# Performance work log

Measured on AMD Instinct MI355X. Metric: run time of the kernel, lower is better.

Reference implementation:

```python
import jax, jax.numpy as jnp
import numpy as np

N_KERNELS = 5
MUL_FACTOR = 2.0


def setup_inputs() -> dict:
    key = jax.random.key(0)
    k1, k2 = jax.random.split(key)
    x = jax.random.normal(k1, (8192, 64), dtype=jnp.float32)
    y = jax.random.normal(k2, (8192, 64), dtype=jnp.float32)
    return {"x": x, "y": y}


def reference(x, y):
    # bandwidth multipliers: mul_factor ** (arange(n) - n//2) -> [0.25,0.5,1,2,4]
    mults = MUL_FACTOR ** (jnp.arange(N_KERNELS, dtype=jnp.float32) - N_KERNELS // 2)

    z = jnp.concatenate([x, y], axis=0)  # [N, d], N = n + m
    n = x.shape[0]
    N = z.shape[0]

    # squared pairwise L2 distances: ||a||^2 + ||b||^2 - 2 a.b, clamped at 0
    sq = jnp.sum(z * z, axis=-1)  # [N]
    d2 = jnp.maximum(sq[:, None] + sq[None, :] - 2.0 * (z @ z.T), 0.0)  # [N, N]

    # data-dependent bandwidth: sum(d2) / (N^2 - N)
    bw = jnp.sum(d2) / (N * N - N)

    # multi-bandwidth RBF kernel, summed over kernels: [N, N]
    K = jnp.sum(jnp.exp(-d2[None, :, :] / (bw * mults)[:, None, None]), axis=0)

    XX = jnp.mean(K[:n, :n])
    XY = jnp.mean(K[:n, n:])
    YY = jnp.mean(K[n:, n:])
    return XX - 2.0 * XY + YY
```

## Files before the change

### kernel.cpp

```cpp
#include <hip/hip_runtime.h>
#include <hip/hip_bf16.h>

#define D 64

typedef __attribute__((ext_vector_type(8))) _Float16 half8;
typedef __attribute__((ext_vector_type(4))) float floatx4;
typedef __attribute__((ext_vector_type(2))) float f32x2;

typedef __attribute__((address_space(1))) unsigned int gu32_t;
typedef __attribute__((address_space(3))) unsigned int lu32_t;

__global__ __launch_bounds__(256) void k_pre(const float* __restrict__ x, const float* __restrict__ y,
                                             int nx, _Float16* __restrict__ zh,
                                             float* __restrict__ sq, double* __restrict__ Tpart,
                                             float* __restrict__ Spart) {
    int tid = threadIdx.x;
    int lane = tid & 63, wid = tid >> 6;
    int t = blockIdx.x * 256 + tid;
    size_t e = (size_t)t * 8;
    int row = (int)(e >> 6);
    const float* src = (row < nx) ? (x + e) : (y + (e - (size_t)nx * D));
    float4 v0 = ((const float4*)src)[0];
    float4 v1 = ((const float4*)src)[1];
    half8 h;
    h[0]=(_Float16)v0.x; h[1]=(_Float16)v0.y; h[2]=(_Float16)v0.z; h[3]=(_Float16)v0.w;
    h[4]=(_Float16)v1.x; h[5]=(_Float16)v1.y; h[6]=(_Float16)v1.z; h[7]=(_Float16)v1.w;
    *(half8*)(zh + e) = h;
    float p = v0.x*v0.x + v0.y*v0.y + v0.z*v0.z + v0.w*v0.w
            + v1.x*v1.x + v1.y*v1.y + v1.z*v1.z + v1.w*v1.w;
    float s = p;
    s += __shfl_xor(s, 1);
    s += __shfl_xor(s, 2);
    s += __shfl_xor(s, 4);
    if ((tid & 7) == 0) sq[row] = s;

    __shared__ float colbuf[32][64];
    int rib = tid >> 3, cg = tid & 7;
    *(float4*)&colbuf[rib][cg * 8]     = v0;
    *(float4*)&colbuf[rib][cg * 8 + 4] = v1;

    double dp = (double)p;
    dp += __shfl_xor(dp, 1);
    dp += __shfl_xor(dp, 2);
    dp += __shfl_xor(dp, 4);
    dp += __shfl_xor(dp, 8);
    dp += __shfl_xor(dp, 16);
    dp += __shfl_xor(dp, 32);
    __shared__ double redw[4];
    if (lane == 0) redw[wid] = dp;
    __syncthreads();
    if (tid == 0) Tpart[blockIdx.x] = (redw[0] + redw[1]) + (redw[2] + redw[3]);

    if (tid < 64) {
        float cs = 0.f;
#pragma unroll
        for (int r2 = 0; r2 < 32; ++r2) cs += colbuf[r2][tid];
        Spart[blockIdx.x * 64 + tid] = cs;
    }
}

__global__ __launch_bounds__(256) void k_bw(const double* __restrict__ Tpart, int ntp,
                                            const float* __restrict__ Spart, int nsp,
                                            int N, float* __restrict__ cq_p) {
    int t = threadIdx.x;
    double Tp = 0.0;
    for (int b = t; b < ntp; b += 256) Tp += Tpart[b];

    int q = t >> 6, col = t & 63;
    int bpq = nsp >> 2;
    const float* sp = Spart + (size_t)(q * bpq) * 64 + col;
    float c0 = 0.f, c1 = 0.f, c2 = 0.f, c3 = 0.f;
    for (int b = 0; b < bpq; b += 4) {
        c0 += sp[(b + 0) * 64];
        c1 += sp[(b + 1) * 64];
        c2 += sp[(b + 2) * 64];
        c3 += sp[(b + 3) * 64];
    }
    __shared__ float cred[256];
    cred[t] = (c0 + c1) + (c2 + c3);

    __shared__ double red[256];
    red[t] = Tp;
    __syncthreads();
    for (int off = 128; off > 0; off >>= 1) {
        if (t < off) red[t] += red[t + off];
        __syncthreads();
    }
    double T = red[0];
    __shared__ double red2[64];
    if (t < 64) {
        float Sk = cred[t] + cred[t + 64] + cred[t + 128] + cred[t + 192];
        red2[t] = (double)Sk * (double)Sk;
    }
    __syncthreads();
    if (t == 0) {
        double S2 = 0.0;
        for (int i = 0; i < 64; ++i) S2 += red2[i];
        double sumd2 = 2.0 * (double)N * T - 2.0 * S2;
        double bw = sumd2 / ((double)N * (double)N - (double)N);
        cq_p[0] = (float)(1.4426950408889634 / (4.0 * bw));
    }
}

__global__ __launch_bounds__(256, 6) void k_mmd(const _Float16* __restrict__ zh,
                                                const float* __restrict__ sq,
                                                const float* __restrict__ cq_p,
                                                int nb, double* __restrict__ partial) {
    int bid = (nb - 1) - (int)blockIdx.x;
    int g = (int)((sqrtf(1.0f + 2.0f * (float)bid) - 1.0f) * 0.5f);
    while (2 * (g + 1) * (g + 2) <= bid) ++g;
    while (2 * g * (g + 1) > bid) --g;
    int r = bid - 2 * g * (g + 1);
    int gp1 = g + 1;
    int rig = r / gp1;
    int jc  = r - rig * gp1;
    int ib  = 4 * g + rig;

    int jstart = jc * 512;
    int jend   = (ib + 1) * 128;
    if (jend > jstart + 512) jend = jstart + 512;
    int nt = (jend - jstart) >> 6;
    int diag_j = ib * 128;

    int tid  = threadIdx.x;
    int lane = tid & 63;
    int wid  = tid >> 6;
    int i0 = ib * 128 + wid * 32;

    float cq  = cq_p[0];
    f32x2 c2q2 = {2.0f * cq, 2.0f * cq};

    int lrow = lane & 15;
    int c2   = lane >> 4;
    int kb   = c2 * 8;

    const _Float16* ar0 = zh + (size_t)(i0 + lrow) * D + kb;
    half8 a00 = *(const half8*)(ar0);
    half8 a01 = *(const half8*)(ar0 + 32);
    half8 a10 = *(const half8*)(ar0 + 16 * D);
    half8 a11 = *(const half8*)(ar0 + 16 * D + 32);

    int irh = c2 * 4;
    f32x2 na[4];
    na[0] = (f32x2){-sq[i0 + irh + 0] * cq, -sq[i0 + irh + 1] * cq};
    na[1] = (f32x2){-sq[i0 + irh + 2] * cq, -sq[i0 + irh + 3] * cq};
    na[2] = (f32x2){-sq[i0 + 16 + irh + 0] * cq, -sq[i0 + 16 + irh + 1] * cq};
    na[3] = (f32x2){-sq[i0 + 16 + irh + 2] * cq, -sq[i0 + 16 + irh + 3] * cq};

    __shared__ __align__(16) _Float16 bsm[2][64 * 64];
    int srow = tid >> 3;
    int scc  = tid & 7;
    int sc   = scc ^ (srow & 7);
    const char* zbase = (const char*)zh + (size_t)jstart * 128 + srow * 128 + sc * 16;
    char* ldsw = (char*)&bsm[0][0] + wid * 1024;

    auto STAGE = [&](int buf, int tile) {
        const char* src = zbase + (size_t)tile * (64 * 128);
        char* dst = ldsw + buf * 8192;
        __builtin_amdgcn_global_load_lds((const gu32_t*)(const void*)src,
                                         (lu32_t*)(void*)dst, 16, 0, 0);
        __builtin_amdgcn_global_load_lds((const gu32_t*)(const void*)(src + 32 * 128),
                                         (lu32_t*)(void*)(dst + 4096), 16, 0, 0);
    };

    float acc = 0.f;

    STAGE(0, 0);
    __syncthreads();

    for (int t = 0; t < nt; ++t) {
        if (t + 1 < nt) STAGE((t + 1) & 1, t + 1);
        const char* bb = (const char*)&bsm[t & 1][0];
        int j0t = jstart + t * 64;
#pragma unroll
        for (int s = 0; s < 4; ++s) {
            int jr = s * 16 + lrow;
            int swz = jr & 7;
            half8 b0 = *(const half8*)(bb + jr * 128 + ((c2 ^ swz) * 16));
            half8 b1 = *(const half8*)(bb + jr * 128 + (((c2 + 4) ^ swz) * 16));
            float sqj = sq[j0t + s * 16 + lrow];

            floatx4 d0 = {0.f, 0.f, 0.f, 0.f};
            floatx4 d1 = {0.f, 0.f, 0.f, 0.f};
            d0 = __builtin_amdgcn_mfma_f32_16x16x32_f16(a00, b0, d0, 0, 0, 0);
            d0 = __builtin_amdgcn_mfma_f32_16x16x32_f16(a01, b1, d0, 0, 0, 0);
            d1 = __builtin_amdgcn_mfma_f32_16x16x32_f16(a10, b0, d1, 0, 0, 0);
            d1 = __builtin_amdgcn_mfma_f32_16x16x32_f16(a11, b1, d1, 0, 0, 0);

            float nbj = -sqj * cq;
            f32x2 nb2 = {nbj, nbj};

            f32x2 dd[4];
            dd[0] = (f32x2){d0[0], d0[1]};
            dd[1] = (f32x2){d0[2], d0[3]};
            dd[2] = (f32x2){d1[0], d1[1]};
            dd[3] = (f32x2){d1[2], d1[3]};

            f32x2 part2 = {0.f, 0.f};
#pragma unroll
            for (int pk = 0; pk < 4; ++pk) {
                f32x2 u = dd[pk] * c2q2 + (na[pk] + nb2);
                u.x = fminf(u.x, 0.f);
                u.y = fminf(u.y, 0.f);
                f32x2 q;
                q.x = __builtin_amdgcn_exp2f(u.x);
                q.y = __builtin_amdgcn_exp2f(u.y);
                f32x2 m1 = q * q;
                f32x2 m2 = m1 * m1;
                f32x2 m3 = m2 * m2;
                part2 += ((q + m1) + (m2 + m3)) + m3 * m3;
            }
            float wf = ((j0t + s * 16) >= diag_j) ? 1.0f : 2.0f;
            acc = fmaf(part2.x + part2.y, wf, acc);
        }
        __syncthreads();
    }

    double wacc = (double)acc;
    wacc += __shfl_xor(wacc, 1);
    wacc += __shfl_xor(wacc, 2);
    wacc += __shfl_xor(wacc, 4);
    wacc += __shfl_xor(wacc, 8);
    wacc += __shfl_xor(wacc, 16);
    wacc += __shfl_xor(wacc, 32);
    __shared__ double redr[4];
    if (lane == 0) redr[wid] = wacc;
    __syncthreads();
    if (tid == 0) partial[bid] = (redr[0] + redr[1]) + (redr[2] + redr[3]);
}

__global__ __launch_bounds__(256) void k_final(const double* __restrict__ partial, int nb,
                                               int nxTile, int nxChunk,
                                               int nx, int ny, float* __restrict__ out) {
    int t = threadIdx.x;
    double sXX = 0.0, sXY = 0.0, sYY = 0.0;
    for (int p = t; p < nb; p += 256) {
        int g = (int)((sqrtf(1.0f + 2.0f * (float)p) - 1.0f) * 0.5f);
        while (2 * (g + 1) * (g + 2) <= p) ++g;
        while (2 * g * (g + 1) > p) --g;
        int r = p - 2 * g * (g + 1);
        int gp1 = g + 1;
        int rig = r / gp1;
        int jc  = r - rig * gp1;
        int ib  = 4 * g + rig;
        double v = partial[p];
        bool iX = ib < nxTile;
        bool jX = jc < nxChunk;
        if (iX && jX) sXX += v;
        else if (iX != jX) sXY += v;
        else sYY += v;
    }
    __shared__ double r0[256], r1[256], r2[256];
    r0[t] = sXX; r1[t] = sXY; r2[t] = sYY;
    __syncthreads();
    for (int off = 128; off > 0; off >>= 1) {
        if (t < off) {
            r0[t] += r0[t + off];
            r1[t] += r1[t + off];
            r2[t] += r2[t + off];
        }
        __syncthreads();
    }
    if (t == 0) {
        double XX = r0[0] / ((double)nx * (double)nx);
        double XY = r1[0] / (2.0 * (double)nx * (double)ny);
        double YY = r2[0] / ((double)ny * (double)ny);
        out[0] = (float)(XX - 2.0 * XY + YY);
    }
}

extern "C" void kernel_launch(void* const* d_in, const int* in_sizes, int n_in,
                              void* d_out, int out_size, void* d_ws, size_t ws_size,
                              hipStream_t stream) {
    const float* x = (const float*)d_in[0];
    const float* y = (const float*)d_in[1];
    float* out = (float*)d_out;

    int nx = in_sizes[0] / D;
    int ny = in_sizes[1] / D;
    int N  = nx + ny;

    int pre_blocks = (N * D / 8) / 256;
    int nT = N / 128;
    int ngr = nT / 4;
    int nb = 2 * ngr * (ngr + 1);
    int nxTile = nx / 128;
    int nxChunk = nx / 512;

    char* w = (char*)d_ws;
    double* Tpart   = (double*)(w + 0);
    double* partial = (double*)(w + 4096);
    float*  Spart   = (float*) (w + 20992);
    float*  sq      = (float*) (w + 152064);
    float*  cq      = (float*) (w + 217600);
    _Float16* zh    = (_Float16*)(w + 217664);

    k_pre   <<<pre_blocks, 256, 0, stream>>>(x, y, nx, zh, sq, Tpart, Spart);
    k_bw    <<<1, 256, 0, stream>>>(Tpart, pre_blocks, Spart, pre_blocks, N, cq);
    k_mmd   <<<nb, 256, 0, stream>>>(zh, sq, cq, nb, partial);
    k_final <<<1, 256, 0, stream>>>(partial, nb, nxTile, nxChunk, nx, ny, out);
}
```

Before: 127.2 us.

## Make each wave an independent job with private LDS triple-step pipeline

Reworks the pairwise-distance kernel so each wavefront owns its own 32-row strip job with a private double-buffered LDS slice. This removes block-wide __syncthreads and the cross-wave reduction. Loads for tile t+2 are issued after reading tile t, with an explicit vmcnt wait in place of barriers. The triangular job mapping is recomputed at finer granularity, and the occupancy hint drops from 6 to 5. Each wave now loads its own B tiles instead of sharing them, so global/L2 traffic rises. The final kernel also hardcodes the split at 256 strips and 16 chunks, which only holds for nx=8192.

Measured after the change: 142.6 us. 1.12x slower.

```diff
diff --git a/kernel.cpp b/kernel.cpp
--- a/kernel.cpp
+++ b/kernel.cpp
@@ -102,39 +102,37 @@
     }
 }
 
-__global__ __launch_bounds__(256, 6) void k_mmd(const _Float16* __restrict__ zh,
+__global__ __launch_bounds__(256, 5) void k_mmd(const _Float16* __restrict__ zh,
                                                 const float* __restrict__ sq,
                                                 const float* __restrict__ cq_p,
-                                                int nb, double* __restrict__ partial) {
-    int bid = (nb - 1) - (int)blockIdx.x;
-    int g = (int)((sqrtf(1.0f + 2.0f * (float)bid) - 1.0f) * 0.5f);
-    while (2 * (g + 1) * (g + 2) <= bid) ++g;
-    while (2 * g * (g + 1) > bid) --g;
-    int r = bid - 2 * g * (g + 1);
-    int gp1 = g + 1;
-    int rig = r / gp1;
-    int jc  = r - rig * gp1;
-    int ib  = 4 * g + rig;
-
-    int jstart = jc * 512;
-    int jend   = (ib + 1) * 128;
-    if (jend > jstart + 512) jend = jstart + 512;
-    int nt = (jend - jstart) >> 6;
-    int diag_j = ib * 128;
-
+                                                int njobs, double* __restrict__ partial) {
     int tid  = threadIdx.x;
     int lane = tid & 63;
     int wid  = tid >> 6;
-    int i0 = ib * 128 + wid * 32;
+    int J = (njobs - 1) - ((int)blockIdx.x * 4 + wid);
+
+    int m = (int)((1.0f + sqrtf(1.0f + 0.5f * (float)J)) * 0.5f);
+    if (m < 1) m = 1;
+    while (8 * m * (m + 1) <= J) ++m;
+    while (8 * m * (m - 1) > J) --m;
+    int r   = J - 8 * m * (m - 1);
+    int sig = r / m;
+    int c   = r - sig * m;
+    int s   = 16 * (m - 1) + sig;
+
+    int i0 = s * 32;
+    int jstart = c * 512;
+    int width = (s + 1) * 32 - jstart; if (width > 512) width = 512;
+    int nt = width >> 5;
+    int diag_j = i0;
 
     float cq  = cq_p[0];
     f32x2 c2q2 = {2.0f * cq, 2.0f * cq};
 
     int lrow = lane & 15;
     int c2   = lane >> 4;
-    int kb   = c2 * 8;
-
-    const _Float16* ar0 = zh + (size_t)(i0 + lrow) * D + kb;
+
+    const _Float16* ar0 = zh + (size_t)(i0 + lrow) * D + c2 * 8;
     half8 a00 = *(const half8*)(ar0);
     half8 a01 = *(const half8*)(ar0 + 32);
     half8 a10 = *(const half8*)(ar0 + 16 * D);
@@ -147,38 +145,51 @@
     na[2] = (f32x2){-sq[i0 + 16 + irh + 0] * cq, -sq[i0 + 16 + irh + 1] * cq};
     na[3] = (f32x2){-sq[i0 + 16 + irh + 2] * cq, -sq[i0 + 16 + irh + 3] * cq};
 
-    __shared__ __align__(16) _Float16 bsm[2][64 * 64];
-    int srow = tid >> 3;
-    int scc  = tid & 7;
-    int sc   = scc ^ (srow & 7);
-    const char* zbase = (const char*)zh + (size_t)jstart * 128 + srow * 128 + sc * 16;
-    char* ldsw = (char*)&bsm[0][0] + wid * 1024;
-
-    auto STAGE = [&](int buf, int tile) {
-        const char* src = zbase + (size_t)tile * (64 * 128);
-        char* dst = ldsw + buf * 8192;
-        __builtin_amdgcn_global_load_lds((const gu32_t*)(const void*)src,
-                                         (lu32_t*)(void*)dst, 16, 0, 0);
-        __builtin_amdgcn_global_load_lds((const gu32_t*)(const void*)(src + 32 * 128),
-                                         (lu32_t*)(void*)(dst + 4096), 16, 0, 0);
+    __shared__ __align__(16) _Float16 bsm[4][2][32 * 64];
+    char* wbase = (char*)&bsm[wid][0][0];
+    int lr8 = lane >> 3;
+    int lc8 = lane & 7;
+    const char* zlane = (const char*)zh + (size_t)jstart * 128 + lr8 * 128 + ((lc8 ^ lr8) * 16);
+
+    auto STAGE = [&](int buf, int t) {
+        const char* srcb = zlane + (size_t)t * 4096;
+        char* dstb = wbase + buf * 4096;
+#pragma unroll
+        for (int q = 0; q < 4; ++q)
+            __builtin_amdgcn_global_load_lds((const gu32_t*)(const void*)(srcb + q * 1024),
+                                             (lu32_t*)(void*)(dstb + q * 1024), 16, 0, 0);
     };
 
     float acc = 0.f;
 
     STAGE(0, 0);
-    __syncthreads();
+    if (nt > 1) STAGE(1, 1);
 
     for (int t = 0; t < nt; ++t) {
-        if (t + 1 < nt) STAGE((t + 1) & 1, t + 1);
-        const char* bb = (const char*)&bsm[t & 1][0];
-        int j0t = jstart + t * 64;
+        asm volatile("s_waitcnt vmcnt(0)" ::: "memory");
+        __builtin_amdgcn_sched_barrier(0);
+        const char* bb = wbase + (t & 1) * 4096;
+        int j0t = jstart + t * 32;
+
+        half8 b0_0, b1_0, b0_1, b1_1;
+        {
+            int jr0 = lrow,      sw0 = jr0 & 7;
+            int jr1 = 16 + lrow, sw1 = jr1 & 7;
+            b0_0 = *(const half8*)(bb + jr0 * 128 + ((c2 ^ sw0) * 16));
+            b1_0 = *(const half8*)(bb + jr0 * 128 + (((c2 + 4) ^ sw0) * 16));
+            b0_1 = *(const half8*)(bb + jr1 * 128 + ((c2 ^ sw1) * 16));
+            b1_1 = *(const half8*)(bb + jr1 * 128 + (((c2 + 4) ^ sw1) * 16));
+        }
+        float sqj0 = sq[j0t + lrow];
+        float sqj1 = sq[j0t + 16 + lrow];
+        __builtin_amdgcn_sched_barrier(0);
+        if (t + 2 < nt) STAGE(t & 1, t + 2);
+
 #pragma unroll
-        for (int s = 0; s < 4; ++s) {
-            int jr = s * 16 + lrow;
-            int swz = jr & 7;
-            half8 b0 = *(const half8*)(bb + jr * 128 + ((c2 ^ swz) * 16));
-            half8 b1 = *(const half8*)(bb + jr * 128 + (((c2 + 4) ^ swz) * 16));
-            float sqj = sq[j0t + s * 16 + lrow];
+        for (int si = 0; si < 2; ++si) {
+            half8 b0 = si ? b0_1 : b0_0;
+            half8 b1 = si ? b1_1 : b1_0;
+            float sqj = si ? sqj1 : sqj0;
 
             floatx4 d0 = {0.f, 0.f, 0.f, 0.f};
             floatx4 d1 = {0.f, 0.f, 0.f, 0.f};
@@ -189,7 +200,6 @@
 
             float nbj = -sqj * cq;
             f32x2 nb2 = {nbj, nbj};
-
             f32x2 dd[4];
             dd[0] = (f32x2){d0[0], d0[1]};
             dd[1] = (f32x2){d0[2], d0[3]};
@@ -210,10 +220,9 @@
                 f32x2 m3 = m2 * m2;
                 part2 += ((q + m1) + (m2 + m3)) + m3 * m3;
             }
-            float wf = ((j0t + s * 16) >= diag_j) ? 1.0f : 2.0f;
+            float wf = ((j0t + si * 16) >= diag_j) ? 1.0f : 2.0f;
             acc = fmaf(part2.x + part2.y, wf, acc);
         }
-        __syncthreads();
     }
 
     double wacc = (double)acc;
@@ -223,29 +232,25 @@
     wacc += __shfl_xor(wacc, 8);
     wacc += __shfl_xor(wacc, 16);
     wacc += __shfl_xor(wacc, 32);
-    __shared__ double redr[4];
-    if (lane == 0) redr[wid] = wacc;
-    __syncthreads();
-    if (tid == 0) partial[bid] = (redr[0] + redr[1]) + (redr[2] + redr[3]);
-}
-
-__global__ __launch_bounds__(256) void k_final(const double* __restrict__ partial, int nb,
-                                               int nxTile, int nxChunk,
+    if (lane == 0) partial[J] = wacc;
+}
+
+__global__ __launch_bounds__(256) void k_final(const double* __restrict__ partial, int njobs,
                                                int nx, int ny, float* __restrict__ out) {
     int t = threadIdx.x;
     double sXX = 0.0, sXY = 0.0, sYY = 0.0;
-    for (int p = t; p < nb; p += 256) {
-        int g = (int)((sqrtf(1.0f + 2.0f * (float)p) - 1.0f) * 0.5f);
-        while (2 * (g + 1) * (g + 2) <= p) ++g;
-        while (2 * g * (g + 1) > p) --g;
-        int r = p - 2 * g * (g + 1);
-        int gp1 = g + 1;
-        int rig = r / gp1;
-        int jc  = r - rig * gp1;
-        int ib  = 4 * g + rig;
+    for (int p = t; p < njobs; p += 256) {
+        int m = (int)((1.0f + sqrtf(1.0f + 0.5f * (float)p)) * 0.5f);
+        if (m < 1) m = 1;
+        while (8 * m * (m + 1) <= p) ++m;
+        while (8 * m * (m - 1) > p) --m;
+        int r   = p - 8 * m * (m - 1);
+        int sig = r / m;
+        int c   = r - sig * m;
+        int s   = 16 * (m - 1) + sig;
         double v = partial[p];
-        bool iX = ib < nxTile;
-        bool jX = jc < nxChunk;
+        bool iX = s < 256;
+        bool jX = c < 16;
         if (iX && jX) sXX += v;
         else if (iX != jX) sXY += v;
         else sYY += v;
@@ -281,22 +286,21 @@
     int N  = nx + ny;
 
     int pre_blocks = (N * D / 8) / 256;
-    int nT = N / 128;
-    int ngr = nT / 4;
-    int nb = 2 * ngr * (ngr + 1);
-    int nxTile = nx / 128;
-    int nxChunk = nx / 512;
+    int nstrips = N / 32;
+    int M = nstrips / 16;
+    int njobs = 8 * M * (M + 1);
+    int nblk = njobs / 4;
 
     char* w = (char*)d_ws;
     double* Tpart   = (double*)(w + 0);
     double* partial = (double*)(w + 4096);
-    float*  Spart   = (float*) (w + 20992);
-    float*  sq      = (float*) (w + 152064);
-    float*  cq      = (float*) (w + 217600);
-    _Float16* zh    = (_Float16*)(w + 217664);
+    float*  Spart   = (float*) (w + 71680);
+    float*  sq      = (float*) (w + 202752);
+    float*  cq      = (float*) (w + 268288);
+    _Float16* zh    = (_Float16*)(w + 268352);
 
     k_pre   <<<pre_blocks, 256, 0, stream>>>(x, y, nx, zh, sq, Tpart, Spart);
     k_bw    <<<1, 256, 0, stream>>>(Tpart, pre_blocks, Spart, pre_blocks, N, cq);
-    k_mmd   <<<nb, 256, 0, stream>>>(zh, sq, cq, nb, partial);
-    k_final <<<1, 256, 0, stream>>>(partial, nb, nxTile, nxChunk, nx, ny, out);
-}
+    k_mmd   <<<nblk, 256, 0, stream>>>(zh, sq, cq, njobs, partial);
+    k_final <<<1, 256, 0, stream>>>(partial, njobs, nx, ny, out);
+}
```
